# Kernel tuning notes

Measured on AMD Instinct MI355X. Metric: run time of the kernel, lower is better.

The kernel has to match this reference:

```python
import jax, jax.numpy as jnp
import numpy as np

B, C, G = 16384, 30, 7  # YOLOv1: 2 boxes*5 + 20 classes = 30 channels, 7x7 grid


def setup_inputs() -> dict:
    key = jax.random.key(0)
    k1, k2, k3 = jax.random.split(key, 3)
    pred = jax.random.uniform(k1, (B, C, G, G), dtype=jnp.float32)
    labels = jax.random.uniform(k2, (B, C, G, G), dtype=jnp.float32)
    # objectness indicator must be exactly 0.0 or 1.0 (source tests == 1)
    obj = (jax.random.uniform(k3, (B, G, G)) < 0.15).astype(jnp.float32)
    labels = labels.at[:, 4].set(obj)
    return {"pred": pred, "labels": labels}


def _xyxy(px, py, w, h, gx, gy, M, N):
    # (px,py) are cell-relative centers; grid index m along dim -2, n along dim -1
    cx = (px + gx) / M
    cy = (py + gy) / N
    return cx - w / 2, cy - h / 2, cx + w / 2, cy + h / 2


def _iou(a, b):
    x1 = jnp.maximum(a[0], b[0])
    y1 = jnp.maximum(a[1], b[1])
    x2 = jnp.minimum(a[2], b[2])
    y2 = jnp.minimum(a[3], b[3])
    inter = jnp.clip(x2 - x1, 0.0) * jnp.clip(y2 - y1, 0.0)
    area_a = (a[2] - a[0]) * (a[3] - a[1])
    area_b = (b[2] - b[0]) * (b[3] - b[1])
    return jnp.where(inter > 0, inter / (area_a + area_b - inter), 0.0)


def reference(pred, labels):
    M, N = labels.shape[-2], labels.shape[-1]  # num_gridx, num_gridy
    gx = jnp.arange(M, dtype=pred.dtype)[:, None]  # m index (dim -2)
    gy = jnp.arange(N, dtype=pred.dtype)[None, :]  # n index (dim -1)

    b1 = _xyxy(pred[:, 0], pred[:, 1], pred[:, 2], pred[:, 3], gx, gy, M, N)
    b2 = _xyxy(pred[:, 5], pred[:, 6], pred[:, 7], pred[:, 8], gx, gy, M, N)
    bg = _xyxy(labels[:, 0], labels[:, 1], labels[:, 2], labels[:, 3], gx, gy, M, N)

    iou1 = _iou(b1, bg)  # [B, G, G]
    iou2 = _iou(b2, bg)
    resp1 = iou1 > iou2

    obj = (labels[:, 4] == 1.0).astype(pred.dtype)  # [B, G, G]

    coor1 = (jnp.sum((pred[:, 0:2] - labels[:, 0:2]) ** 2, axis=1)
             + jnp.sum((jnp.sqrt(pred[:, 2:4]) - jnp.sqrt(labels[:, 2:4])) ** 2, axis=1))
    coor2 = (jnp.sum((pred[:, 5:7] - labels[:, 5:7]) ** 2, axis=1)
             + jnp.sum((jnp.sqrt(pred[:, 7:9]) - jnp.sqrt(labels[:, 7:9])) ** 2, axis=1))
    coor = jnp.where(resp1, coor1, coor2)

    obj_conf = jnp.where(resp1, (pred[:, 4] - iou1) ** 2, (pred[:, 9] - iou2) ** 2)
    noobj_resp = jnp.where(resp1, (pred[:, 9] - iou2) ** 2, (pred[:, 4] - iou1) ** 2)
    cls = jnp.sum((pred[:, 10:] - labels[:, 10:]) ** 2, axis=1)

    coor_loss = 5.0 * jnp.sum(coor * obj)
    obj_confi_loss = jnp.sum(obj_conf * obj)
    noobj_confi_loss = (0.5 * jnp.sum(noobj_resp * obj)
                        + 0.5 * jnp.sum((pred[:, 4] ** 2 + pred[:, 9] ** 2) * (1.0 - obj)))
    class_loss = jnp.sum(cls * obj)

    loss = coor_loss + obj_confi_loss + noobj_confi_loss + class_loss
    # NOTE: the source shadows `n` (batch size) with the inner grid loop variable,
    # so the final division is by range(7)[-1] == 6, NOT by batch size. Faithful:
    return loss / (N - 1)
```

## Files before the change

kernel.cpp:

```cpp
#include <hip/hip_runtime.h>


constexpr int BATCH  = 16384;
constexpr int CH     = 30;
constexpr int G      = 7;
constexpr int GG     = G * G;
constexpr int TPB    = 256;
constexpr int IPB    = 4;
constexpr int IMG_F  = CH * GG;
constexpr int BLK_F  = IPB * IMG_F;
constexpr int BLK_V4 = BLK_F / 4;
constexpr int NBLK   = BATCH / IPB;
constexpr int FULL_IT = BLK_V4 / TPB;
constexpr int TAIL    = BLK_V4 - FULL_IT * TPB;

__device__ __forceinline__ float sq(float x) { return x * x; }

__global__ __launch_bounds__(TPB) void yolo_loss_partial(
    const float* __restrict__ pred,
    const float* __restrict__ lab,
    float* __restrict__ ws)
{
    __shared__ float4 sp4[BLK_V4];
    __shared__ float4 sl4[BLK_V4];
    __shared__ float wsum[TPB / 64];

    const int t = threadIdx.x;
    const float4* gp = (const float4*)(pred + (size_t)blockIdx.x * BLK_F);
    const float4* gl = (const float4*)(lab  + (size_t)blockIdx.x * BLK_F);

    float4 rp[FULL_IT + 1], rl[FULL_IT + 1];
#pragma unroll
    for (int j = 0; j < FULL_IT; ++j) {
        rp[j] = gp[t + j * TPB];
        rl[j] = gl[t + j * TPB];
    }
    const bool tail = t < TAIL;
    if (tail) {
        rp[FULL_IT] = gp[t + FULL_IT * TPB];
        rl[FULL_IT] = gl[t + FULL_IT * TPB];
    }
#pragma unroll
    for (int j = 0; j < FULL_IT; ++j) {
        sp4[t + j * TPB] = rp[j];
        sl4[t + j * TPB] = rl[j];
    }
    if (tail) {
        sp4[t + FULL_IT * TPB] = rp[FULL_IT];
        sl4[t + FULL_IT * TPB] = rl[FULL_IT];
    }
    __syncthreads();

    const float* sp = (const float*)sp4;
    const float* sl = (const float*)sl4;

    float cell_loss = 0.0f;
    if (t < IPB * GG) {
        const int img  = t / GG;
        const int cell = t - img * GG;
        const int m    = cell / G;
        const int n    = cell - m * G;

        const float* p = sp + img * IMG_F + cell;
        const float* l = sl + img * IMG_F + cell;

        float pv[10];
#pragma unroll
        for (int c = 0; c < 10; ++c) pv[c] = p[c * GG];
        float lv[9];
#pragma unroll
        for (int c = 0; c < 9; ++c) lv[c] = l[c * GG];

        float cls = 0.0f;
#pragma unroll
        for (int c = 10; c < 30; ++c) {
            float d = p[c * GG] - l[c * GG];
            cls += d * d;
        }

        const float gx = (float)m;
        const float gy = (float)n;
        const float inv7 = 1.0f / 7.0f;

        const float cx1 = (pv[0] + gx) * inv7, cy1 = (pv[1] + gy) * inv7;
        const float hw1 = 0.5f * pv[2],        hh1 = 0.5f * pv[3];
        const float a1x1 = cx1 - hw1, a1y1 = cy1 - hh1, a1x2 = cx1 + hw1, a1y2 = cy1 + hh1;
        const float cx2 = (pv[5] + gx) * inv7, cy2 = (pv[6] + gy) * inv7;
        const float hw2 = 0.5f * pv[7],        hh2 = 0.5f * pv[8];
        const float a2x1 = cx2 - hw2, a2y1 = cy2 - hh2, a2x2 = cx2 + hw2, a2y2 = cy2 + hh2;
        const float cxg = (lv[0] + gx) * inv7, cyg = (lv[1] + gy) * inv7;
        const float hwg = 0.5f * lv[2],        hhg = 0.5f * lv[3];
        const float bx1 = cxg - hwg, by1 = cyg - hhg, bx2 = cxg + hwg, by2 = cyg + hhg;

        const float area_g = (bx2 - bx1) * (by2 - by1);

        float ix1 = fmaxf(a1x1, bx1), iy1 = fmaxf(a1y1, by1);
        float ix2 = fminf(a1x2, bx2), iy2 = fminf(a1y2, by2);
        float inter1 = fmaxf(ix2 - ix1, 0.0f) * fmaxf(iy2 - iy1, 0.0f);
        float area1  = (a1x2 - a1x1) * (a1y2 - a1y1);
        float iou1 = (inter1 > 0.0f) ? inter1 / (area1 + area_g - inter1) : 0.0f;

        ix1 = fmaxf(a2x1, bx1); iy1 = fmaxf(a2y1, by1);
        ix2 = fminf(a2x2, bx2); iy2 = fminf(a2y2, by2);
        float inter2 = fmaxf(ix2 - ix1, 0.0f) * fmaxf(iy2 - iy1, 0.0f);
        float area2  = (a2x2 - a2x1) * (a2y2 - a2y1);
        float iou2 = (inter2 > 0.0f) ? inter2 / (area2 + area_g - inter2) : 0.0f;

        const bool resp1 = iou1 > iou2;
        const float obj = (lv[4] == 1.0f) ? 1.0f : 0.0f;

        const float coor1 = sq(pv[0] - lv[0]) + sq(pv[1] - lv[1])
                          + sq(sqrtf(pv[2]) - sqrtf(lv[2])) + sq(sqrtf(pv[3]) - sqrtf(lv[3]));
        const float coor2 = sq(pv[5] - lv[5]) + sq(pv[6] - lv[6])
                          + sq(sqrtf(pv[7]) - sqrtf(lv[7])) + sq(sqrtf(pv[8]) - sqrtf(lv[8]));
        const float coor = resp1 ? coor1 : coor2;

        const float e1 = sq(pv[4] - iou1);
        const float e2 = sq(pv[9] - iou2);
        const float obj_conf   = resp1 ? e1 : e2;
        const float noobj_resp = resp1 ? e2 : e1;

        cell_loss = obj * (5.0f * coor + obj_conf + 0.5f * noobj_resp + cls)
                  + (1.0f - obj) * 0.5f * (pv[4] * pv[4] + pv[9] * pv[9]);
    }

    float v = cell_loss;
#pragma unroll
    for (int off = 32; off > 0; off >>= 1) v += __shfl_down(v, off, 64);

    const int lane = t & 63;
    const int wid  = t >> 6;
    if (lane == 0) wsum[wid] = v;
    __syncthreads();
    if (t == 0) ws[blockIdx.x] = wsum[0] + wsum[1] + wsum[2] + wsum[3];
}

__global__ __launch_bounds__(TPB) void yolo_loss_final(
    const float* __restrict__ ws, float* __restrict__ out)
{
    const int t = threadIdx.x;
    const float4* w4 = (const float4*)ws;
    float4 a = make_float4(0.f, 0.f, 0.f, 0.f);
#pragma unroll
    for (int j = 0; j < NBLK / 4 / TPB; ++j) {
        float4 x = w4[t + j * TPB];
        a.x += x.x; a.y += x.y; a.z += x.z; a.w += x.w;
    }
    float v = (a.x + a.y) + (a.z + a.w);
#pragma unroll
    for (int off = 32; off > 0; off >>= 1) v += __shfl_down(v, off, 64);

    __shared__ float wsum[TPB / 64];
    const int lane = t & 63;
    const int wid  = t >> 6;
    if (lane == 0) wsum[wid] = v;
    __syncthreads();
    if (t == 0) {
        out[0] = (wsum[0] + wsum[1] + wsum[2] + wsum[3]) * (1.0f / 6.0f);
    }
}

extern "C" void kernel_launch(void* const* d_in, const int* in_sizes, int n_in,
                              void* d_out, int out_size, void* d_ws, size_t ws_size,
                              hipStream_t stream) {
    const float* pred = (const float*)d_in[0];
    const float* lab  = (const float*)d_in[1];
    float* ws  = (float*)d_ws;
    float* out = (float*)d_out;

    yolo_loss_partial<<<NBLK, TPB, 0, stream>>>(pred, lab, ws);
    yolo_loss_final<<<1, TPB, 0, stream>>>(ws, out);
}
```

Before: 229.3 us.

## Copy inputs straight to LDS asynchronously and halve images per block

The staging of prediction and label tiles through registers is replaced with `global_load_lds` 16-byte direct-to-LDS copies, so the data skips the VGPR round trip. Images per block also drop from 4 to 2, which halves shared-memory use per block and doubles the number of blocks. Both aim to raise occupancy and memory-level parallelism in this bandwidth-bound reduction. The cost is fewer active compute threads per block and a larger partial-sum array. Correctness also depends on `__syncthreads` waiting for the async LDS writes to finish.

```diff
diff --git a/kernel.cpp b/kernel.cpp
--- a/kernel.cpp
+++ b/kernel.cpp
@@ -6,7 +6,7 @@
 constexpr int G      = 7;
 constexpr int GG     = G * G;
 constexpr int TPB    = 256;
-constexpr int IPB    = 4;
+constexpr int IPB    = 2;
 constexpr int IMG_F  = CH * GG;
 constexpr int BLK_F  = IPB * IMG_F;
 constexpr int BLK_V4 = BLK_F / 4;
@@ -15,6 +15,13 @@
 constexpr int TAIL    = BLK_V4 - FULL_IT * TPB;
 
 __device__ __forceinline__ float sq(float x) { return x * x; }
+
+__device__ __forceinline__ void async_copy16(const float4* gsrc, float4* ldst) {
+    __builtin_amdgcn_global_load_lds(
+        (const __attribute__((address_space(1))) void*)gsrc,
+        (__attribute__((address_space(3))) void*)ldst,
+        16, 0, 0);
+}
 
 __global__ __launch_bounds__(TPB) void yolo_loss_partial(
     const float* __restrict__ pred,
@@ -26,29 +33,21 @@
     __shared__ float wsum[TPB / 64];
 
     const int t = threadIdx.x;
+    const int wbase = t & ~63;
     const float4* gp = (const float4*)(pred + (size_t)blockIdx.x * BLK_F);
     const float4* gl = (const float4*)(lab  + (size_t)blockIdx.x * BLK_F);
 
-    float4 rp[FULL_IT + 1], rl[FULL_IT + 1];
 #pragma unroll
-    for (int j = 0; j < FULL_IT; ++j) {
-        rp[j] = gp[t + j * TPB];
-        rl[j] = gl[t + j * TPB];
-    }
-    const bool tail = t < TAIL;
-    if (tail) {
-        rp[FULL_IT] = gp[t + FULL_IT * TPB];
-        rl[FULL_IT] = gl[t + FULL_IT * TPB];
-    }
+    for (int it = 0; it < FULL_IT; ++it)
+        async_copy16(gp + it * TPB + t, sp4 + it * TPB + wbase);
+    if (t < TAIL)
+        async_copy16(gp + FULL_IT * TPB + t, sp4 + FULL_IT * TPB + wbase);
 #pragma unroll
-    for (int j = 0; j < FULL_IT; ++j) {
-        sp4[t + j * TPB] = rp[j];
-        sl4[t + j * TPB] = rl[j];
-    }
-    if (tail) {
-        sp4[t + FULL_IT * TPB] = rp[FULL_IT];
-        sl4[t + FULL_IT * TPB] = rl[FULL_IT];
-    }
+    for (int it = 0; it < FULL_IT; ++it)
+        async_copy16(gl + it * TPB + t, sl4 + it * TPB + wbase);
+    if (t < TAIL)
+        async_copy16(gl + FULL_IT * TPB + t, sl4 + FULL_IT * TPB + wbase);
+
     __syncthreads();
 
     const float* sp = (const float*)sp4;
```

Measured after the change: 202.6 us, median of 2. -11.7%, faster.

## Stage only box channels in shared memory and stream class channels directly

Applied to the files above, without the earlier changes.

The kernel now handles 8 images per block. Only the first 10 box channels of pred and labels go through shared memory. The 20 class channels are read straight from global memory as float2 and weighted by the objectness value looked up in shared memory, so every thread does useful class-loss work instead of only 49 threads per image. The aim is to cut LDS traffic and footprint and raise thread utilisation, at the cost of float2 rather than float4 loads and some modulo index arithmetic.

```diff
diff --git a/kernel.cpp b/kernel.cpp
--- a/kernel.cpp
+++ b/kernel.cpp
@@ -2,135 +2,162 @@
 
 
 constexpr int BATCH  = 16384;
-constexpr int CH     = 30;
 constexpr int G      = 7;
 constexpr int GG     = G * G;
+constexpr int IMG_F  = 30 * GG;
 constexpr int TPB    = 256;
-constexpr int IPB    = 4;
-constexpr int IMG_F  = CH * GG;
-constexpr int BLK_F  = IPB * IMG_F;
-constexpr int BLK_V4 = BLK_F / 4;
-constexpr int NBLK   = BATCH / IPB;
-constexpr int FULL_IT = BLK_V4 / TPB;
-constexpr int TAIL    = BLK_V4 - FULL_IT * TPB;
+constexpr int NIMG   = 8;
+constexpr int NBLK   = BATCH / NIMG;
+constexpr int BOX_F  = 10 * GG;
+constexpr int BOX_V2 = BOX_F / 2;
+constexpr int IMG_V2 = IMG_F / 2;
+constexpr int CLS_V2 = IMG_V2 - BOX_V2;
+constexpr int STAGE_TOT = 2 * NIMG * BOX_V2;
+constexpr int STAGE_FULL = STAGE_TOT / TPB;
+constexpr int STAGE_TAIL = STAGE_TOT - STAGE_FULL * TPB;
+constexpr int NCELL  = NIMG * GG;
 
 __device__ __forceinline__ float sq(float x) { return x * x; }
+
+__device__ __forceinline__ float cell_box_loss(
+    const float* __restrict__ sp,
+    const float* __restrict__ sl,
+    int cell)
+{
+    const int m = cell / G;
+    const int n = cell - m * G;
+
+    float pv[10];
+#pragma unroll
+    for (int c = 0; c < 10; ++c) pv[c] = sp[c * GG + cell];
+    float lv[9];
+#pragma unroll
+    for (int c = 0; c < 9; ++c) lv[c] = sl[c * GG + cell];
+
+    const float gx = (float)m;
+    const float gy = (float)n;
+    const float inv7 = 1.0f / 7.0f;
+
+    const float cx1 = (pv[0] + gx) * inv7, cy1 = (pv[1] + gy) * inv7;
+    const float hw1 = 0.5f * pv[2],        hh1 = 0.5f * pv[3];
+    const float a1x1 = cx1 - hw1, a1y1 = cy1 - hh1, a1x2 = cx1 + hw1, a1y2 = cy1 + hh1;
+    const float cx2 = (pv[5] + gx) * inv7, cy2 = (pv[6] + gy) * inv7;
+    const float hw2 = 0.5f * pv[7],        hh2 = 0.5f * pv[8];
+    const float a2x1 = cx2 - hw2, a2y1 = cy2 - hh2, a2x2 = cx2 + hw2, a2y2 = cy2 + hh2;
+    const float cxg = (lv[0] + gx) * inv7, cyg = (lv[1] + gy) * inv7;
+    const float hwg = 0.5f * lv[2],        hhg = 0.5f * lv[3];
+    const float bx1 = cxg - hwg, by1 = cyg - hhg, bx2 = cxg + hwg, by2 = cyg + hhg;
+
+    const float area_g = (bx2 - bx1) * (by2 - by1);
+
+    float ix1 = fmaxf(a1x1, bx1), iy1 = fmaxf(a1y1, by1);
+    float ix2 = fminf(a1x2, bx2), iy2 = fminf(a1y2, by2);
+    float inter1 = fmaxf(ix2 - ix1, 0.0f) * fmaxf(iy2 - iy1, 0.0f);
+    float area1  = (a1x2 - a1x1) * (a1y2 - a1y1);
+    float iou1 = (inter1 > 0.0f) ? inter1 / (area1 + area_g - inter1) : 0.0f;
+
+    ix1 = fmaxf(a2x1, bx1); iy1 = fmaxf(a2y1, by1);
+    ix2 = fminf(a2x2, bx2); iy2 = fminf(a2y2, by2);
+    float inter2 = fmaxf(ix2 - ix1, 0.0f) * fmaxf(iy2 - iy1, 0.0f);
+    float area2  = (a2x2 - a2x1) * (a2y2 - a2y1);
+    float iou2 = (inter2 > 0.0f) ? inter2 / (area2 + area_g - inter2) : 0.0f;
+
+    const bool resp1 = iou1 > iou2;
+    const float obj = (lv[4] == 1.0f) ? 1.0f : 0.0f;
+
+    const float coor1 = sq(pv[0] - lv[0]) + sq(pv[1] - lv[1])
+                      + sq(sqrtf(pv[2]) - sqrtf(lv[2])) + sq(sqrtf(pv[3]) - sqrtf(lv[3]));
+    const float coor2 = sq(pv[5] - lv[5]) + sq(pv[6] - lv[6])
+                      + sq(sqrtf(pv[7]) - sqrtf(lv[7])) + sq(sqrtf(pv[8]) - sqrtf(lv[8]));
+    const float coor = resp1 ? coor1 : coor2;
+
+    const float e1 = sq(pv[4] - iou1);
+    const float e2 = sq(pv[9] - iou2);
+    const float obj_conf   = resp1 ? e1 : e2;
+    const float noobj_resp = resp1 ? e2 : e1;
+
+    return obj * (5.0f * coor + obj_conf + 0.5f * noobj_resp)
+         + (1.0f - obj) * 0.5f * (pv[4] * pv[4] + pv[9] * pv[9]);
+}
 
 __global__ __launch_bounds__(TPB) void yolo_loss_partial(
     const float* __restrict__ pred,
     const float* __restrict__ lab,
     float* __restrict__ ws)
 {
-    __shared__ float4 sp4[BLK_V4];
-    __shared__ float4 sl4[BLK_V4];
+    __shared__ float sbox_p[NIMG][BOX_F];
+    __shared__ float sbox_l[NIMG][BOX_F];
     __shared__ float wsum[TPB / 64];
 
     const int t = threadIdx.x;
-    const float4* gp = (const float4*)(pred + (size_t)blockIdx.x * BLK_F);
-    const float4* gl = (const float4*)(lab  + (size_t)blockIdx.x * BLK_F);
-
-    float4 rp[FULL_IT + 1], rl[FULL_IT + 1];
-#pragma unroll
-    for (int j = 0; j < FULL_IT; ++j) {
-        rp[j] = gp[t + j * TPB];
-        rl[j] = gl[t + j * TPB];
-    }
-    const bool tail = t < TAIL;
-    if (tail) {
-        rp[FULL_IT] = gp[t + FULL_IT * TPB];
-        rl[FULL_IT] = gl[t + FULL_IT * TPB];
-    }
-#pragma unroll
-    for (int j = 0; j < FULL_IT; ++j) {
-        sp4[t + j * TPB] = rp[j];
-        sl4[t + j * TPB] = rl[j];
-    }
-    if (tail) {
-        sp4[t + FULL_IT * TPB] = rp[FULL_IT];
-        sl4[t + FULL_IT * TPB] = rl[FULL_IT];
+    const size_t blk_f = (size_t)blockIdx.x * NIMG * IMG_F;
+    const float2* gp2 = (const float2*)(pred + blk_f);
+    const float2* gl2 = (const float2*)(lab  + blk_f);
+
+#pragma unroll
+    for (int it = 0; it <= STAGE_FULL; ++it) {
+        const int j = t + it * TPB;
+        if (it < STAGE_FULL || t < STAGE_TAIL) {
+            const int is_l  = j >= NIMG * BOX_V2;
+            const int local = j - is_l * (NIMG * BOX_V2);
+            const int img   = local / BOX_V2;
+            const int k     = local - img * BOX_V2;
+            const float2 v = (is_l ? gl2 : gp2)[img * IMG_V2 + k];
+            float* dst = (is_l ? &sbox_l[img][2 * k] : &sbox_p[img][2 * k]);
+            *(float2*)dst = v;
+        }
     }
     __syncthreads();
 
-    const float* sp = (const float*)sp4;
-    const float* sl = (const float*)sl4;
-
-    float cell_loss = 0.0f;
-    if (t < IPB * GG) {
+    float acc = 0.0f;
+
+#pragma unroll
+    for (int i = 0; i < NIMG; ++i) {
+        const float2* pc = gp2 + i * IMG_V2 + BOX_V2;
+        const float2* lc = gl2 + i * IMG_V2 + BOX_V2;
+        const float* objp = &sbox_l[i][4 * GG];
+        {
+            const float2 p = pc[t], l = lc[t];
+            const int n0 = 2 * t;
+            const int c0 = n0 % 49;
+            const int c1 = (c0 == 48) ? 0 : c0 + 1;
+            const float w0 = (objp[c0] == 1.0f) ? 1.0f : 0.0f;
+            const float w1 = (objp[c1] == 1.0f) ? 1.0f : 0.0f;
+            const float d0 = p.x - l.x, d1 = p.y - l.y;
+            acc += w0 * d0 * d0 + w1 * d1 * d1;
+        }
+        if (t < CLS_V2 - TPB) {
+            const int u = t + TPB;
+            const float2 p = pc[u], l = lc[u];
+            const int n0 = 2 * u;
+            const int c0 = n0 % 49;
+            const int c1 = (c0 == 48) ? 0 : c0 + 1;
+            const float w0 = (objp[c0] == 1.0f) ? 1.0f : 0.0f;
+            const float w1 = (objp[c1] == 1.0f) ? 1.0f : 0.0f;
+            const float d0 = p.x - l.x, d1 = p.y - l.y;
+            acc += w0 * d0 * d0 + w1 * d1 * d1;
+        }
+    }
+
+    {
         const int img  = t / GG;
         const int cell = t - img * GG;
-        const int m    = cell / G;
-        const int n    = cell - m * G;
-
-        const float* p = sp + img * IMG_F + cell;
-        const float* l = sl + img * IMG_F + cell;
-
-        float pv[10];
-#pragma unroll
-        for (int c = 0; c < 10; ++c) pv[c] = p[c * GG];
-        float lv[9];
-#pragma unroll
-        for (int c = 0; c < 9; ++c) lv[c] = l[c * GG];
-
-        float cls = 0.0f;
-#pragma unroll
-        for (int c = 10; c < 30; ++c) {
-            float d = p[c * GG] - l[c * GG];
-            cls += d * d;
-        }
-
-        const float gx = (float)m;
-        const float gy = (float)n;
-        const float inv7 = 1.0f / 7.0f;
-
-        const float cx1 = (pv[0] + gx) * inv7, cy1 = (pv[1] + gy) * inv7;
-        const float hw1 = 0.5f * pv[2],        hh1 = 0.5f * pv[3];
-        const float a1x1 = cx1 - hw1, a1y1 = cy1 - hh1, a1x2 = cx1 + hw1, a1y2 = cy1 + hh1;
-        const float cx2 = (pv[5] + gx) * inv7, cy2 = (pv[6] + gy) * inv7;
-        const float hw2 = 0.5f * pv[7],        hh2 = 0.5f * pv[8];
-        const float a2x1 = cx2 - hw2, a2y1 = cy2 - hh2, a2x2 = cx2 + hw2, a2y2 = cy2 + hh2;
-        const float cxg = (lv[0] + gx) * inv7, cyg = (lv[1] + gy) * inv7;
-        const float hwg = 0.5f * lv[2],        hhg = 0.5f * lv[3];
-        const float bx1 = cxg - hwg, by1 = cyg - hhg, bx2 = cxg + hwg, by2 = cyg + hhg;
-
-        const float area_g = (bx2 - bx1) * (by2 - by1);
-
-        float ix1 = fmaxf(a1x1, bx1), iy1 = fmaxf(a1y1, by1);
-        float ix2 = fminf(a1x2, bx2), iy2 = fminf(a1y2, by2);
-        float inter1 = fmaxf(ix2 - ix1, 0.0f) * fmaxf(iy2 - iy1, 0.0f);
-        float area1  = (a1x2 - a1x1) * (a1y2 - a1y1);
-        float iou1 = (inter1 > 0.0f) ? inter1 / (area1 + area_g - inter1) : 0.0f;
-
-        ix1 = fmaxf(a2x1, bx1); iy1 = fmaxf(a2y1, by1);
-        ix2 = fminf(a2x2, bx2); iy2 = fminf(a2y2, by2);
-        float inter2 = fmaxf(ix2 - ix1, 0.0f) * fmaxf(iy2 - iy1, 0.0f);
-        float area2  = (a2x2 - a2x1) * (a2y2 - a2y1);
-        float iou2 = (inter2 > 0.0f) ? inter2 / (area2 + area_g - inter2) : 0.0f;
-
-        const bool resp1 = iou1 > iou2;
-        const float obj = (lv[4] == 1.0f) ? 1.0f : 0.0f;
-
-        const float coor1 = sq(pv[0] - lv[0]) + sq(pv[1] - lv[1])
-                          + sq(sqrtf(pv[2]) - sqrtf(lv[2])) + sq(sqrtf(pv[3]) - sqrtf(lv[3]));
-        const float coor2 = sq(pv[5] - lv[5]) + sq(pv[6] - lv[6])
-                          + sq(sqrtf(pv[7]) - sqrtf(lv[7])) + sq(sqrtf(pv[8]) - sqrtf(lv[8]));
-        const float coor = resp1 ? coor1 : coor2;
-
-        const float e1 = sq(pv[4] - iou1);
-        const float e2 = sq(pv[9] - iou2);
-        const float obj_conf   = resp1 ? e1 : e2;
-        const float noobj_resp = resp1 ? e2 : e1;
-
-        cell_loss = obj * (5.0f * coor + obj_conf + 0.5f * noobj_resp + cls)
-                  + (1.0f - obj) * 0.5f * (pv[4] * pv[4] + pv[9] * pv[9]);
-    }
-
-    float v = cell_loss;
-#pragma unroll
-    for (int off = 32; off > 0; off >>= 1) v += __shfl_down(v, off, 64);
+        if (t < NCELL)
+            acc += cell_box_loss(sbox_p[img], sbox_l[img], cell);
+    }
+    if (t < NCELL - TPB) {
+        const int u    = t + TPB;
+        const int img  = u / GG;
+        const int cell = u - img * GG;
+        acc += cell_box_loss(sbox_p[img], sbox_l[img], cell);
+    }
+
+#pragma unroll
+    for (int off = 32; off > 0; off >>= 1) acc += __shfl_down(acc, off, 64);
 
     const int lane = t & 63;
     const int wid  = t >> 6;
-    if (lane == 0) wsum[wid] = v;
+    if (lane == 0) wsum[wid] = acc;
     __syncthreads();
     if (t == 0) ws[blockIdx.x] = wsum[0] + wsum[1] + wsum[2] + wsum[3];
 }
```

Result: faster. 209.6 us (-8.6%).

## Stream class channels through registers and stage only box channels in LDS

Applied to the files above, without the earlier changes.

Each wave now handles two images and streams their float4 data straight from global memory. The 20 class channels are reduced on the fly in registers, weighted by an objectness mask staged up front. Only the 10 predicted and 8 label box channels go to shared memory for the per-cell IoU math. This cuts LDS use per image, which raises occupancy and removes the full-tile LDS round trip. In exchange it adds per-element index arithmetic, an extra pass to read objectness, and divergent branches.

```diff
diff --git a/kernel.cpp b/kernel.cpp
--- a/kernel.cpp
+++ b/kernel.cpp
@@ -1,18 +1,20 @@
 #include <hip/hip_runtime.h>
 
 
-constexpr int BATCH  = 16384;
-constexpr int CH     = 30;
-constexpr int G      = 7;
-constexpr int GG     = G * G;
-constexpr int TPB    = 256;
-constexpr int IPB    = 4;
-constexpr int IMG_F  = CH * GG;
-constexpr int BLK_F  = IPB * IMG_F;
-constexpr int BLK_V4 = BLK_F / 4;
-constexpr int NBLK   = BATCH / IPB;
-constexpr int FULL_IT = BLK_V4 / TPB;
-constexpr int TAIL    = BLK_V4 - FULL_IT * TPB;
+constexpr int BATCH   = 16384;
+constexpr int G       = 7;
+constexpr int GG      = 49;
+constexpr int IMG_F   = 30 * GG;
+constexpr int TPB     = 256;
+constexpr int WAVES   = TPB / 64;
+constexpr int IPW     = 2;
+constexpr int IPB     = WAVES * IPW;
+constexpr int NBLK    = BATCH / IPB;
+constexpr int SPAN_F  = IPW * IMG_F;
+constexpr int SPAN_V4 = SPAN_F / 4;
+constexpr int NIT     = (SPAN_V4 + 63) / 64;
+constexpr int CHUNK   = 6;
+constexpr int NCHUNK  = NIT / CHUNK;
 
 __device__ __forceinline__ float sq(float x) { return x * x; }
 
@@ -21,116 +23,138 @@
     const float* __restrict__ lab,
     float* __restrict__ ws)
 {
-    __shared__ float4 sp4[BLK_V4];
-    __shared__ float4 sl4[BLK_V4];
-    __shared__ float wsum[TPB / 64];
+    __shared__ float obj_s[IPB * GG];
+    __shared__ float box_p[IPB * 10 * GG];
+    __shared__ float box_l[IPB * 8  * GG];
+    __shared__ float wsum[WAVES];
 
-    const int t = threadIdx.x;
-    const float4* gp = (const float4*)(pred + (size_t)blockIdx.x * BLK_F);
-    const float4* gl = (const float4*)(lab  + (size_t)blockIdx.x * BLK_F);
+    const int t    = threadIdx.x;
+    const int lane = t & 63;
+    const int wid  = t >> 6;
+    const size_t blk_f = (size_t)blockIdx.x * IPB * IMG_F;
 
-    float4 rp[FULL_IT + 1], rl[FULL_IT + 1];
-#pragma unroll
-    for (int j = 0; j < FULL_IT; ++j) {
-        rp[j] = gp[t + j * TPB];
-        rl[j] = gl[t + j * TPB];
-    }
-    const bool tail = t < TAIL;
-    if (tail) {
-        rp[FULL_IT] = gp[t + FULL_IT * TPB];
-        rl[FULL_IT] = gl[t + FULL_IT * TPB];
-    }
-#pragma unroll
-    for (int j = 0; j < FULL_IT; ++j) {
-        sp4[t + j * TPB] = rp[j];
-        sl4[t + j * TPB] = rl[j];
-    }
-    if (tail) {
-        sp4[t + FULL_IT * TPB] = rp[FULL_IT];
-        sl4[t + FULL_IT * TPB] = rl[FULL_IT];
+    for (int j = t; j < IPB * GG; j += TPB) {
+        const int im   = j / GG;
+        const int cell = j - im * GG;
+        const float v  = lab[blk_f + (size_t)im * IMG_F + 4 * GG + cell];
+        obj_s[j] = (v == 1.0f) ? 1.0f : 0.0f;
     }
     __syncthreads();
 
-    const float* sp = (const float*)sp4;
-    const float* sl = (const float*)sl4;
+    const int wimg = wid * IPW;
+    const float4* P4 = (const float4*)(pred + blk_f + wid * SPAN_F);
+    const float4* L4 = (const float4*)(lab  + blk_f + wid * SPAN_F);
 
-    float cell_loss = 0.0f;
-    if (t < IPB * GG) {
-        const int img  = t / GG;
-        const int cell = t - img * GG;
-        const int m    = cell / G;
-        const int n    = cell - m * G;
+    float acc = 0.0f;
 
-        const float* p = sp + img * IMG_F + cell;
-        const float* l = sl + img * IMG_F + cell;
+    for (int chk = 0; chk < NCHUNK; ++chk) {
+        float4 pp[CHUNK], ll[CHUNK];
+        int   id[CHUNK];
+        bool  vd[CHUNK];
+#pragma unroll
+        for (int j = 0; j < CHUNK; ++j) {
+            const int idx = lane + 64 * (chk * CHUNK + j);
+            vd[j] = idx < SPAN_V4;
+            id[j] = vd[j] ? idx : 0;
+            pp[j] = P4[id[j]];
+            ll[j] = L4[id[j]];
+        }
+#pragma unroll
+        for (int j = 0; j < CHUNK; ++j) {
+            const int e0 = id[j] * 4;
+            const float pq[4] = {pp[j].x, pp[j].y, pp[j].z, pp[j].w};
+            const float lq[4] = {ll[j].x, ll[j].y, ll[j].z, ll[j].w};
+#pragma unroll
+            for (int q = 0; q < 4; ++q) {
+                const int e    = e0 + q;
+                const int im   = (e >= IMG_F) ? 1 : 0;
+                const int r    = e - im * IMG_F;
+                const int c    = r / GG;
+                const int cell = r - c * GG;
+                const int I    = wimg + im;
+                if (c >= 10) {
+                    const float w = obj_s[I * GG + cell];
+                    const float d = pq[q] - lq[q];
+                    acc += w * d * d;
+                } else if (vd[j]) {
+                    box_p[I * (10 * GG) + r] = pq[q];
+                    if (c != 4 && c != 9) {
+                        const int rl = r - ((c >= 5) ? GG : 0);
+                        box_l[I * (8 * GG) + rl] = lq[q];
+                    }
+                }
+            }
+        }
+    }
+    __syncthreads();
 
-        float pv[10];
+    if (lane < GG) {
 #pragma unroll
-        for (int c = 0; c < 10; ++c) pv[c] = p[c * GG];
-        float lv[9];
+        for (int im = 0; im < IPW; ++im) {
+            const int I = wimg + im;
+            const float* bp = &box_p[I * (10 * GG)];
+            const float* bl = &box_l[I * (8 * GG)];
+
+            float pv[10];
 #pragma unroll
-        for (int c = 0; c < 9; ++c) lv[c] = l[c * GG];
+            for (int c = 0; c < 10; ++c) pv[c] = bp[c * GG + lane];
+            const float lv0 = bl[0 * GG + lane], lv1 = bl[1 * GG + lane];
+            const float lv2 = bl[2 * GG + lane], lv3 = bl[3 * GG + lane];
+            const float lv5 = bl[4 * GG + lane], lv6 = bl[5 * GG + lane];
+            const float lv7 = bl[6 * GG + lane], lv8 = bl[7 * GG + lane];
+            const float obj = obj_s[I * GG + lane];
 
-        float cls = 0.0f;
-#pragma unroll
-        for (int c = 10; c < 30; ++c) {
-            float d = p[c * GG] - l[c * GG];
-            cls += d * d;
+            const int m = lane / G;
+            const int n = lane - m * G;
+            const float gx = (float)m, gy = (float)n;
+            const float inv7 = 1.0f / 7.0f;
+
+            const float cx1 = (pv[0] + gx) * inv7, cy1 = (pv[1] + gy) * inv7;
+            const float hw1 = 0.5f * pv[2],        hh1 = 0.5f * pv[3];
+            const float a1x1 = cx1 - hw1, a1y1 = cy1 - hh1, a1x2 = cx1 + hw1, a1y2 = cy1 + hh1;
+            const float cx2 = (pv[5] + gx) * inv7, cy2 = (pv[6] + gy) * inv7;
+            const float hw2 = 0.5f * pv[7],        hh2 = 0.5f * pv[8];
+            const float a2x1 = cx2 - hw2, a2y1 = cy2 - hh2, a2x2 = cx2 + hw2, a2y2 = cy2 + hh2;
+            const float cxg = (lv0 + gx) * inv7,   cyg = (lv1 + gy) * inv7;
+            const float hwg = 0.5f * lv2,          hhg = 0.5f * lv3;
+            const float bx1 = cxg - hwg, by1 = cyg - hhg, bx2 = cxg + hwg, by2 = cyg + hhg;
+
+            const float area_g = (bx2 - bx1) * (by2 - by1);
+
+            float ix1 = fmaxf(a1x1, bx1), iy1 = fmaxf(a1y1, by1);
+            float ix2 = fminf(a1x2, bx2), iy2 = fminf(a1y2, by2);
+            float inter1 = fmaxf(ix2 - ix1, 0.0f) * fmaxf(iy2 - iy1, 0.0f);
+            float area1  = (a1x2 - a1x1) * (a1y2 - a1y1);
+            float iou1 = (inter1 > 0.0f) ? inter1 / (area1 + area_g - inter1) : 0.0f;
+
+            ix1 = fmaxf(a2x1, bx1); iy1 = fmaxf(a2y1, by1);
+            ix2 = fminf(a2x2, bx2); iy2 = fminf(a2y2, by2);
+            float inter2 = fmaxf(ix2 - ix1, 0.0f) * fmaxf(iy2 - iy1, 0.0f);
+            float area2  = (a2x2 - a2x1) * (a2y2 - a2y1);
+            float iou2 = (inter2 > 0.0f) ? inter2 / (area2 + area_g - inter2) : 0.0f;
+
+            const bool resp1 = iou1 > iou2;
+
+            const float coor1 = sq(pv[0] - lv0) + sq(pv[1] - lv1)
+                              + sq(sqrtf(pv[2]) - sqrtf(lv2)) + sq(sqrtf(pv[3]) - sqrtf(lv3));
+            const float coor2 = sq(pv[5] - lv5) + sq(pv[6] - lv6)
+                              + sq(sqrtf(pv[7]) - sqrtf(lv7)) + sq(sqrtf(pv[8]) - sqrtf(lv8));
+            const float coor = resp1 ? coor1 : coor2;
+
+            const float e1 = sq(pv[4] - iou1);
+            const float e2 = sq(pv[9] - iou2);
+            const float obj_conf   = resp1 ? e1 : e2;
+            const float noobj_resp = resp1 ? e2 : e1;
+
+            acc += obj * (5.0f * coor + obj_conf + 0.5f * noobj_resp)
+                 + (1.0f - obj) * 0.5f * (pv[4] * pv[4] + pv[9] * pv[9]);
         }
-
-        const float gx = (float)m;
-        const float gy = (float)n;
-        const float inv7 = 1.0f / 7.0f;
-
-        const float cx1 = (pv[0] + gx) * inv7, cy1 = (pv[1] + gy) * inv7;
-        const float hw1 = 0.5f * pv[2],        hh1 = 0.5f * pv[3];
-        const float a1x1 = cx1 - hw1, a1y1 = cy1 - hh1, a1x2 = cx1 + hw1, a1y2 = cy1 + hh1;
-        const float cx2 = (pv[5] + gx) * inv7, cy2 = (pv[6] + gy) * inv7;
-        const float hw2 = 0.5f * pv[7],        hh2 = 0.5f * pv[8];
-        const float a2x1 = cx2 - hw2, a2y1 = cy2 - hh2, a2x2 = cx2 + hw2, a2y2 = cy2 + hh2;
-        const float cxg = (lv[0] + gx) * inv7, cyg = (lv[1] + gy) * inv7;
-        const float hwg = 0.5f * lv[2],        hhg = 0.5f * lv[3];
-        const float bx1 = cxg - hwg, by1 = cyg - hhg, bx2 = cxg + hwg, by2 = cyg + hhg;
-
-        const float area_g = (bx2 - bx1) * (by2 - by1);
-
-        float ix1 = fmaxf(a1x1, bx1), iy1 = fmaxf(a1y1, by1);
-        float ix2 = fminf(a1x2, bx2), iy2 = fminf(a1y2, by2);
-        float inter1 = fmaxf(ix2 - ix1, 0.0f) * fmaxf(iy2 - iy1, 0.0f);
-        float area1  = (a1x2 - a1x1) * (a1y2 - a1y1);
-        float iou1 = (inter1 > 0.0f) ? inter1 / (area1 + area_g - inter1) : 0.0f;
-
-        ix1 = fmaxf(a2x1, bx1); iy1 = fmaxf(a2y1, by1);
-        ix2 = fminf(a2x2, bx2); iy2 = fminf(a2y2, by2);
-        float inter2 = fmaxf(ix2 - ix1, 0.0f) * fmaxf(iy2 - iy1, 0.0f);
-        float area2  = (a2x2 - a2x1) * (a2y2 - a2y1);
-        float iou2 = (inter2 > 0.0f) ? inter2 / (area2 + area_g - inter2) : 0.0f;
-
-        const bool resp1 = iou1 > iou2;
-        const float obj = (lv[4] == 1.0f) ? 1.0f : 0.0f;
-
-        const float coor1 = sq(pv[0] - lv[0]) + sq(pv[1] - lv[1])
-                          + sq(sqrtf(pv[2]) - sqrtf(lv[2])) + sq(sqrtf(pv[3]) - sqrtf(lv[3]));
-        const float coor2 = sq(pv[5] - lv[5]) + sq(pv[6] - lv[6])
-                          + sq(sqrtf(pv[7]) - sqrtf(lv[7])) + sq(sqrtf(pv[8]) - sqrtf(lv[8]));
-        const float coor = resp1 ? coor1 : coor2;
-
-        const float e1 = sq(pv[4] - iou1);
-        const float e2 = sq(pv[9] - iou2);
-        const float obj_conf   = resp1 ? e1 : e2;
-        const float noobj_resp = resp1 ? e2 : e1;
-
-        cell_loss = obj * (5.0f * coor + obj_conf + 0.5f * noobj_resp + cls)
-                  + (1.0f - obj) * 0.5f * (pv[4] * pv[4] + pv[9] * pv[9]);
     }
 
-    float v = cell_loss;
 #pragma unroll
-    for (int off = 32; off > 0; off >>= 1) v += __shfl_down(v, off, 64);
+    for (int off = 32; off > 0; off >>= 1) acc += __shfl_down(acc, off, 64);
 
-    const int lane = t & 63;
-    const int wid  = t >> 6;
-    if (lane == 0) wsum[wid] = v;
+    if (lane == 0) wsum[wid] = acc;
     __syncthreads();
     if (t == 0) ws[blockIdx.x] = wsum[0] + wsum[1] + wsum[2] + wsum[3];
 }
```

Measured after the change: 210.4 us. -8.3%, faster.
